# Performance work log

Hardware: AMD Instinct MI355X
Metric: run time of the kernel (lower is better)

The kernel has to match this reference:

```python
import jax, jax.numpy as jnp
import numpy as np

B, T, DIM = 2, 4096, 2048
H, HKV = 16, 4
HD = DIM // H          # 128
NREP = H // HKV        # 4
R = 16                 # csa_compress_ratio
TOPK = 64              # min(csa_top_k, max_seq_len // R)
THETA = 10000.0


def setup_inputs() -> dict:
    key = jax.random.key(0)
    ks = jax.random.split(key, 9)
    s = 0.02
    return {
        "x":   jax.random.normal(ks[0], (B, T, DIM), jnp.float32),
        "wq":  jax.random.normal(ks[1], (DIM, H * HD),  jnp.float32) * s,
        "wk":  jax.random.normal(ks[2], (DIM, HKV * HD), jnp.float32) * s,
        "wv":  jax.random.normal(ks[3], (DIM, HKV * HD), jnp.float32) * s,
        "wo":  jax.random.normal(ks[4], (DIM, DIM), jnp.float32) * s,
        "wiq": jax.random.normal(ks[5], (DIM, HD), jnp.float32) * s,
        "wik": jax.random.normal(ks[6], (DIM, HD), jnp.float32) * s,
        "cwa": jax.random.normal(ks[7], (HD,), jnp.float32) * s,
        "cwb": jax.random.normal(ks[8], (HD,), jnp.float32) * s,
    }


def _rope(x, cos, sin):
    # x: [B, h, T, HD]; pairs (x[2i], x[2i+1]) rotated by angle[t, i]
    half = HD // 2
    xr = x.reshape(*x.shape[:-1], half, 2)
    a, b = xr[..., 0], xr[..., 1]          # [B, h, T, half]
    ra = a * cos - b * sin                 # cos/sin: [T, half] broadcast
    rb = a * sin + b * cos
    return jnp.stack([ra, rb], axis=-1).reshape(x.shape)


def reference(x, wq, wk, wv, wo, wiq, wik, cwa, cwb):
    Bx, Tx, C = x.shape
    half = HD // 2
    # RoPE tables (buffer in original, deterministic -> recomputed here)
    freqs = 1.0 / (THETA ** (jnp.arange(half, dtype=jnp.float32) / half))
    ang = jnp.arange(Tx, dtype=jnp.float32)[:, None] * freqs[None, :]  # [T, half]
    cos, sin = jnp.cos(ang), jnp.sin(ang)

    q = (x @ wq).reshape(Bx, Tx, H, HD).transpose(0, 2, 1, 3)    # [B,H,T,HD]
    k = (x @ wk).reshape(Bx, Tx, HKV, HD).transpose(0, 2, 1, 3)  # [B,HKV,T,HD]
    v = (x @ wv).reshape(Bx, Tx, HKV, HD).transpose(0, 2, 1, 3)
    q = _rope(q, cos, sin)
    k = _rope(k, cos, sin)

    # chunked softmax-weighted KV compression (vectorized over blocks)
    nb = Tx // R
    kb = k.reshape(Bx, HKV, nb, R, HD)
    vb = v.reshape(Bx, HKV, nb, R, HD)
    wa = jax.nn.softmax(kb @ cwa, axis=-1)   # [B,HKV,nb,R], softmax within block
    wb_ = jax.nn.softmax(kb @ cwb, axis=-1)
    w = 0.5 * (wa + wb_)
    ck = jnp.einsum('bhnr,bhnrd->bhnd', w, kb)  # [B,HKV,nb,HD]
    cv = jnp.einsum('bhnr,bhnrd->bhnd', w, vb)

    # indexer: scores[b,t] = mean_j( qi[b,t] . ki[b,j] ) = qi[b,t] . mean_j ki[b,j]
    qi = x @ wiq                         # [B,T,HD]
    ki_mean = (x @ wik).mean(axis=1)     # [B,HD]
    scores = jnp.einsum('btd,bd->bt', qi, ki_mean)  # [B,T]
    block_scores = scores[:, :nb]                   # [B,nb]

    if nb > TOPK:
        idx = jax.lax.top_k(block_scores, TOPK)[1]             # [B,TOPK]
        ck = jnp.take_along_axis(ck, idx[:, None, :, None], axis=2)  # [B,HKV,TOPK,HD]
        cv = jnp.take_along_axis(cv, idx[:, None, :, None], axis=2)

    # GQA repeat + sparse attention over selected compressed blocks (no mask)
    k_rep = jnp.repeat(ck, NREP, axis=1)   # [B,H,TOPK,HD]
    v_rep = jnp.repeat(cv, NREP, axis=1)
    att = jax.nn.softmax(
        jnp.einsum('bhtd,bhsd->bhts', q, k_rep) / jnp.sqrt(jnp.float32(HD)),
        axis=-1)                            # [B,H,T,TOPK]
    out = jnp.einsum('bhts,bhsd->bhtd', att, v_rep)
    out = out.transpose(0, 2, 1, 3).reshape(Bx, Tx, C)
    return out @ wo
```

## Files before the change

### kernel.cpp

```cpp
#include <hip/hip_runtime.h>
#include <math.h>
#include <stdint.h>

#define BB    2
#define TT    4096
#define CDIM  2048
#define NHQ   16
#define NKV   4
#define HD    128
#define HALF  64
#define NREP  4
#define RBLK  16
#define NB    256
#define TOPK  64

#define MROWS (BB * TT)
#define NQKV  (CDIM + 2 * NKV * HD)
#define XELE  ((size_t)MROWS * CDIM)

typedef __bf16 bf16;
typedef __bf16 bf16x4 __attribute__((ext_vector_type(4)));
typedef __bf16 bf16x8 __attribute__((ext_vector_type(8)));
typedef float f32x4 __attribute__((ext_vector_type(4)));

typedef __attribute__((address_space(1))) unsigned int gu32;
typedef __attribute__((address_space(3))) unsigned int lu32;

__device__ __forceinline__ void gload_lds16(const void* g, void* l) {
  void* gv = const_cast<void*>(g);
  __builtin_amdgcn_global_load_lds((gu32*)gv, (lu32*)l, 16, 0, 0);
}


#define LDS_BUF 24576
#define OFF_AL  8192
#define OFF_BH  16384
#define OFF_BL  20480

__device__ __forceinline__ void mfma3_step(const bf16* __restrict__ sb, int arow,
                                           int brow, int chunk, f32x4 acc[4][4]) {
  bf16x8 fah[4], fal[4], fbh[4], fbl[4];
#pragma unroll
  for (int i = 0; i < 4; ++i) {
    fah[i] = *(const bf16x8*)&sb[(arow + i * 16) * 32 + chunk];
    fal[i] = *(const bf16x8*)&sb[OFF_AL + (arow + i * 16) * 32 + chunk];
  }
#pragma unroll
  for (int j = 0; j < 4; ++j) {
    fbh[j] = *(const bf16x8*)&sb[OFF_BH + (brow + j * 16) * 32 + chunk];
    fbl[j] = *(const bf16x8*)&sb[OFF_BL + (brow + j * 16) * 32 + chunk];
  }
  __builtin_amdgcn_s_setprio(1);
#pragma unroll
  for (int j = 0; j < 4; ++j)
#pragma unroll
    for (int i = 0; i < 4; ++i) {
      acc[i][j] = __builtin_amdgcn_mfma_f32_16x16x32_bf16(fah[i], fbh[j], acc[i][j], 0, 0, 0);
      acc[i][j] = __builtin_amdgcn_mfma_f32_16x16x32_bf16(fah[i], fbl[j], acc[i][j], 0, 0, 0);
      acc[i][j] = __builtin_amdgcn_mfma_f32_16x16x32_bf16(fal[i], fbh[j], acc[i][j], 0, 0, 0);
    }
  __builtin_amdgcn_s_setprio(0);
}

__device__ __forceinline__ void mfma3_core8(const bf16* __restrict__ Ah,
                                            const bf16* __restrict__ Al,
                                            const bf16* __restrict__ Bh,
                                            const bf16* __restrict__ Bl,
                                            int bm, int bn,
                                            f32x4 acc[4][4]) {
  __shared__ __align__(16) bf16 smem[2 * LDS_BUF];
  const int tid = threadIdx.x;
  const int wave = tid >> 6, lane = tid & 63;
  const int lr4 = lane >> 2;
  const int cgs = (lane & 3) ^ ((lane >> 3) & 3);
  const size_t stageoff = (size_t)lr4 * CDIM + cgs * 8;

  const bf16* gp[6];
  int loff[6];
#pragma unroll
  for (int u = 0; u < 6; ++u) {
    int c = wave * 6 + u;
    const bf16* base;
    int lbase;
    if (c < 16)      { base = Ah + (size_t)(bm + c * 16) * CDIM;        lbase = c * 512; }
    else if (c < 32) { base = Al + (size_t)(bm + (c - 16) * 16) * CDIM; lbase = OFF_AL + (c - 16) * 512; }
    else if (c < 40) { base = Bh + (size_t)(bn + (c - 32) * 16) * CDIM; lbase = OFF_BH + (c - 32) * 512; }
    else             { base = Bl + (size_t)(bn + (c - 40) * 16) * CDIM; lbase = OFF_BL + (c - 40) * 512; }
    gp[u] = base + stageoff;
    loff[u] = lbase;
  }

  const int wr = wave >> 1, wc = wave & 1;
  const int fr = lane & 15, lg = lane >> 4;
  const int chunk = (lg ^ ((fr >> 1) & 3)) << 3;
  const int arow = wr * 64 + fr;
  const int brow = wc * 64 + fr;

#pragma unroll
  for (int u = 0; u < 6; ++u) gload_lds16(gp[u], &smem[loff[u]]);

  for (int t = 0; t < 63; ++t) {
    const int nbase = ((t + 1) & 1) * LDS_BUF;
    const int kk = (t + 1) * 32;
#pragma unroll
    for (int u = 0; u < 6; ++u) gload_lds16(gp[u] + kk, &smem[nbase + loff[u]]);
    asm volatile("s_waitcnt vmcnt(6)" ::: "memory");
    __builtin_amdgcn_s_barrier();
    asm volatile("" ::: "memory");

    mfma3_step(&smem[(t & 1) * LDS_BUF], arow, brow, chunk, acc);

    asm volatile("" ::: "memory");
    __builtin_amdgcn_s_barrier();
  }
  asm volatile("s_waitcnt vmcnt(0)" ::: "memory");
  __builtin_amdgcn_s_barrier();
  asm volatile("" ::: "memory");
  mfma3_step(&smem[LDS_BUF], arow, brow, chunk, acc);
}

__global__ __launch_bounds__(512, 2) void csa_gemm_qkv(const bf16* __restrict__ xh,
                                                       const bf16* __restrict__ xl,
                                                       const bf16* __restrict__ wth,
                                                       const bf16* __restrict__ wtl,
                                                       float* __restrict__ qb,
                                                       float* __restrict__ kb,
                                                       float* __restrict__ vb) {
  f32x4 acc[4][4] = {};
  const int bm = blockIdx.y << 8, bn = blockIdx.x << 7;
  mfma3_core8(xh, xl, wth, wtl, bm, bn, acc);
  const int wave = threadIdx.x >> 6, lane = threadIdx.x & 63;
  const int wr = wave >> 1, wc = wave & 1;
  const int fr = lane & 15, lg = lane >> 4;
  float* dst; int ncols, colofs;
  if (bn < CDIM)            { dst = qb; ncols = CDIM; colofs = bn; }
  else if (bn < CDIM + 512) { dst = kb; ncols = 512;  colofs = bn - CDIM; }
  else                      { dst = vb; ncols = 512;  colofs = bn - CDIM - 512; }
#pragma unroll
  for (int i = 0; i < 4; ++i)
#pragma unroll
    for (int j = 0; j < 4; ++j) {
      int row0 = bm + wr * 64 + i * 16 + (lg << 2);
      int col = colofs + wc * 64 + j * 16 + fr;
#pragma unroll
      for (int r = 0; r < 4; ++r)
        dst[(size_t)(row0 + r) * ncols + col] = acc[i][j][r];
    }
}

__global__ __launch_bounds__(512, 2) void csa_gemm_wo(const bf16* __restrict__ ah,
                                                      const bf16* __restrict__ al,
                                                      const bf16* __restrict__ wth,
                                                      const bf16* __restrict__ wtl,
                                                      float* __restrict__ C) {
  f32x4 acc[4][4] = {};
  const int bm = blockIdx.y << 8, bn = blockIdx.x << 7;
  mfma3_core8(ah, al, wth, wtl, bm, bn, acc);
  const int wave = threadIdx.x >> 6, lane = threadIdx.x & 63;
  const int wr = wave >> 1, wc = wave & 1;
  const int fr = lane & 15, lg = lane >> 4;
#pragma unroll
  for (int i = 0; i < 4; ++i)
#pragma unroll
    for (int j = 0; j < 4; ++j) {
      int row0 = bm + wr * 64 + i * 16 + (lg << 2);
      int col = bn + wc * 64 + j * 16 + fr;
#pragma unroll
      for (int r = 0; r < 4; ++r)
        C[(size_t)(row0 + r) * CDIM + col] = acc[i][j][r];
    }
}

__global__ void csa_xconv(const float4* __restrict__ x, bf16x4* __restrict__ xh,
                          bf16x4* __restrict__ xl) {
  int i = blockIdx.x * 256 + threadIdx.x;
  float4 v = x[i];
  bf16x4 h, l;
  h[0] = (bf16)v.x; l[0] = (bf16)(v.x - (float)h[0]);
  h[1] = (bf16)v.y; l[1] = (bf16)(v.y - (float)h[1]);
  h[2] = (bf16)v.z; l[2] = (bf16)(v.z - (float)h[2]);
  h[3] = (bf16)v.w; l[3] = (bf16)(v.w - (float)h[3]);
  xh[i] = h;
  xl[i] = l;
}

__global__ __launch_bounds__(256) void csa_wconv(const float* __restrict__ W, int N,
                                                 bf16* __restrict__ wth,
                                                 bf16* __restrict__ wtl, int rowofs) {
  __shared__ float tile[32][33];
  int k0 = blockIdx.y * 32, n0 = blockIdx.x * 32;
  int tx = threadIdx.x & 31, ty = threadIdx.x >> 5;
#pragma unroll
  for (int r = 0; r < 32; r += 8)
    tile[ty + r][tx] = W[(size_t)(k0 + ty + r) * N + n0 + tx];
  __syncthreads();
#pragma unroll
  for (int r = 0; r < 32; r += 8) {
    int n = ty + r;
    float x = tile[tx][n];
    bf16 h = (bf16)x;
    bf16 l = (bf16)(x - (float)h);
    size_t o = (size_t)(rowofs + n0 + n) * CDIM + k0 + tx;
    wth[o] = h;
    wtl[o] = l;
  }
}

__global__ void csa_rope_table(float* __restrict__ cost, float* __restrict__ sint) {
  int idx = blockIdx.x * blockDim.x + threadIdx.x;
  if (idx >= TT * HALF) return;
  int t = idx / HALF, i = idx % HALF;
  double freq = pow(10000.0, -(double)i / (double)HALF);
  double ang = (double)t * freq;
  cost[idx] = (float)cos(ang);
  sint[idx] = (float)sin(ang);
}

__global__ void csa_rope_apply(float* __restrict__ buf, const float* __restrict__ cost,
                               const float* __restrict__ sint, int nheads, int total) {
  int idx = blockIdx.x * blockDim.x + threadIdx.x;
  if (idx >= total) return;
  int i = idx % HALF;
  int h = (idx / HALF) % nheads;
  int t = (idx / (HALF * nheads)) % TT;
  int b = idx / (HALF * nheads * TT);
  float c = cost[t * HALF + i], s = sint[t * HALF + i];
  float* p = buf + ((((size_t)b * TT + t) * nheads + h) * HD) + 2 * i;
  float a = p[0], q = p[1];
  p[0] = a * c - q * s;
  p[1] = a * s + q * c;
}

__global__ void csa_xpart(const float* __restrict__ x, float* __restrict__ xpart) {
  int d = blockIdx.x * 256 + threadIdx.x;
  int ts = blockIdx.y;
  int b = blockIdx.z;
  float s = 0.f;
  int t0 = ts * (TT / 16);
  for (int t = t0; t < t0 + TT / 16; ++t) s += x[((size_t)b * TT + t) * CDIM + d];
  xpart[((size_t)b * 16 + ts) * CDIM + d] = s;
}

__global__ void csa_kimean(const float* __restrict__ xpart, const float* __restrict__ wik,
                           float* __restrict__ ki) {
  int b = blockIdx.x >> 7;
  int j = blockIdx.x & 127;
  int tid = threadIdx.x;
  float s = 0.f;
  for (int d = tid; d < CDIM; d += 256) {
    float xm = 0.f;
#pragma unroll
    for (int ts = 0; ts < 16; ++ts) xm += xpart[((size_t)b * 16 + ts) * CDIM + d];
    s += xm * wik[(size_t)d * HD + j];
  }
  __shared__ float red[256];
  red[tid] = s;
  __syncthreads();
  for (int off = 128; off > 0; off >>= 1) {
    if (tid < off) red[tid] += red[tid + off];
    __syncthreads();
  }
  if (tid == 0) ki[b * HD + j] = red[0] * (1.f / (float)TT);
}

__global__ void csa_u(const float* __restrict__ wiq, const float* __restrict__ ki,
                      float* __restrict__ u) {
  int idx = blockIdx.x * 256 + threadIdx.x;
  int b = idx / CDIM, d = idx % CDIM;
  float s = 0.f;
#pragma unroll 8
  for (int j = 0; j < HD; ++j) s += wiq[(size_t)d * HD + j] * ki[b * HD + j];
  u[idx] = s;
}

__global__ void csa_scores(const float* __restrict__ x, const float* __restrict__ u,
                           float* __restrict__ sc) {
  int b = blockIdx.x >> 8;
  int t = blockIdx.x & 255;
  int tid = threadIdx.x;
  float s = 0.f;
  for (int d = tid; d < CDIM; d += 256)
    s += x[((size_t)b * TT + t) * CDIM + d] * u[b * CDIM + d];
  __shared__ float red[256];
  red[tid] = s;
  __syncthreads();
  for (int off = 128; off > 0; off >>= 1) {
    if (tid < off) red[tid] += red[tid + off];
    __syncthreads();
  }
  if (tid == 0) sc[blockIdx.x] = red[0];
}

__global__ void csa_topk(const float* __restrict__ sc, int* __restrict__ topk) {
  __shared__ float val[NB];
  __shared__ float rv[256];
  __shared__ int ri[256];
  int b = blockIdx.x, tid = threadIdx.x;
  val[tid] = sc[b * NB + tid];
  __syncthreads();
  for (int it = 0; it < TOPK; ++it) {
    rv[tid] = val[tid];
    ri[tid] = tid;
    __syncthreads();
    for (int off = 128; off > 0; off >>= 1) {
      if (tid < off) {
        if (rv[tid + off] > rv[tid] ||
            (rv[tid + off] == rv[tid] && ri[tid + off] < ri[tid])) {
          rv[tid] = rv[tid + off];
          ri[tid] = ri[tid + off];
        }
      }
      __syncthreads();
    }
    if (tid == 0) {
      topk[b * TOPK + it] = ri[0];
      val[ri[0]] = -INFINITY;
    }
    __syncthreads();
  }
}

__global__ __launch_bounds__(64) void csa_compress(const float* __restrict__ kbuf,
                                                   const float* __restrict__ vbuf,
                                                   const int* __restrict__ topk,
                                                   const float* __restrict__ cwa,
                                                   const float* __restrict__ cwb,
                                                   bf16* __restrict__ ckh,
                                                   bf16* __restrict__ ckl,
                                                   bf16* __restrict__ cvth,
                                                   bf16* __restrict__ cvtl) {
  int blk = blockIdx.x;
  int b = blk / (NKV * TOPK);
  int h = (blk / TOPK) % NKV;
  int j = blk % TOPK;
  int n = topk[b * TOPK + j];
  int l = threadIdx.x;
  float ca0 = cwa[l], ca1 = cwa[l + 64];
  float cb0 = cwb[l], cb1 = cwb[l + 64];
  float kk[RBLK][2], vv[RBLK][2], ar[RBLK], br[RBLK];
#pragma unroll
  for (int r = 0; r < RBLK; ++r) {
    int t = n * RBLK + r;
    size_t base = (((size_t)b * TT + t) * NKV + h) * HD;
    kk[r][0] = kbuf[base + l];
    kk[r][1] = kbuf[base + l + 64];
    vv[r][0] = vbuf[base + l];
    vv[r][1] = vbuf[base + l + 64];
    float pa = kk[r][0] * ca0 + kk[r][1] * ca1;
    float pb = kk[r][0] * cb0 + kk[r][1] * cb1;
    for (int off = 32; off > 0; off >>= 1) {
      pa += __shfl_xor(pa, off);
      pb += __shfl_xor(pb, off);
    }
    ar[r] = pa;
    br[r] = pb;
  }
  float ma = -INFINITY, mb = -INFINITY;
#pragma unroll
  for (int r = 0; r < RBLK; ++r) { ma = fmaxf(ma, ar[r]); mb = fmaxf(mb, br[r]); }
  float ea[RBLK], eb[RBLK], sa = 0.f, sb = 0.f;
#pragma unroll
  for (int r = 0; r < RBLK; ++r) {
    ea[r] = expf(ar[r] - ma); sa += ea[r];
    eb[r] = expf(br[r] - mb); sb += eb[r];
  }
  float isa = 1.f / sa, isb = 1.f / sb;
  float o0 = 0.f, o1 = 0.f, p0 = 0.f, p1 = 0.f;
#pragma unroll
  for (int r = 0; r < RBLK; ++r) {
    float w = 0.5f * (ea[r] * isa + eb[r] * isb);
    o0 += w * kk[r][0]; o1 += w * kk[r][1];
    p0 += w * vv[r][0]; p1 += w * vv[r][1];
  }
  size_t ckbase = ((size_t)(b * NKV + h) * 64 + j) * 128;
  bf16 h0 = (bf16)o0; ckh[ckbase + l] = h0;      ckl[ckbase + l] = (bf16)(o0 - (float)h0);
  bf16 h1 = (bf16)o1; ckh[ckbase + l + 64] = h1; ckl[ckbase + l + 64] = (bf16)(o1 - (float)h1);
  size_t vtbase = (size_t)(b * NKV + h) * (128 * 64);
  bf16 g0 = (bf16)p0; cvth[vtbase + (size_t)l * 64 + j] = g0;
  cvtl[vtbase + (size_t)l * 64 + j] = (bf16)(p0 - (float)g0);
  bf16 g1 = (bf16)p1; cvth[vtbase + (size_t)(l + 64) * 64 + j] = g1;
  cvtl[vtbase + (size_t)(l + 64) * 64 + j] = (bf16)(p1 - (float)g1);
}

__global__ __launch_bounds__(256) void csa_attn_mfma(const float* __restrict__ qb,
                                                     const float* __restrict__ cost,
                                                     const float* __restrict__ sint,
                                                     const bf16* __restrict__ ckh_g,
                                                     const bf16* __restrict__ ckl_g,
                                                     const bf16* __restrict__ cvth_g,
                                                     const bf16* __restrict__ cvtl_g,
                                                     bf16* __restrict__ oh_g,
                                                     bf16* __restrict__ ol_g) {
  __shared__ __align__(16) bf16 sck[2][64 * 128];
  __shared__ __align__(16) bf16 sV[2][64 * 64];
  const int tid = threadIdx.x;
  const int wave = tid >> 6, lane = tid & 63;
  const int b = blockIdx.y >> 2, kvh = blockIdx.y & 3;
  const int row0 = blockIdx.x << 7;
  const int wrow = wave << 5;
  const int lr = lane & 15, lg = lane >> 4;
  const float scale = 0.08838834764831845f;

  const bf16* gkh = ckh_g + (size_t)(b * NKV + kvh) * (64 * 128);
  const bf16* gkl = ckl_g + (size_t)(b * NKV + kvh) * (64 * 128);
  const bf16* gvh = cvth_g + (size_t)(b * NKV + kvh) * (128 * 64);
  const bf16* gvl = cvtl_g + (size_t)(b * NKV + kvh) * (128 * 64);

  for (int idx = tid; idx < 1024; idx += 256) {
    int j = idx >> 4, c = idx & 15;
    int dst = (j * 16 + (c ^ (j & 15))) * 8;
    *(uint4*)&sck[0][dst] = *(const uint4*)(gkh + j * 128 + c * 8);
    *(uint4*)&sck[1][dst] = *(const uint4*)(gkl + j * 128 + c * 8);
  }
  for (int idx = tid; idx < 512; idx += 256) {
    int d = idx >> 3, c = idx & 7;
    int dst = (d * 8 + (c ^ (d & 7))) * 8;
    *(uint4*)&sV[0][dst] = *(const uint4*)(gvh + d * 64 + c * 8);
    *(uint4*)&sV[1][dst] = *(const uint4*)(gvl + d * 64 + c * 8);
  }

  bf16x8 qfh[2][4], qfl[2][4];
#pragma unroll
  for (int it = 0; it < 2; ++it)
#pragma unroll
    for (int ks = 0; ks < 4; ++ks) {
      int row = wrow + it * 16 + lr;
      int g = row0 + row;
      int t = g >> 2;
      int hh = kvh * NREP + (g & 3);
      int d0 = ks * 32 + (lg << 3);
      const float* qp = qb + (((size_t)b * TT + t) * NHQ + hh) * HD + d0;
      float4 a = *(const float4*)qp;
      float4 b4 = *(const float4*)(qp + 4);
      float4 cs = *(const float4*)&cost[t * HALF + (d0 >> 1)];
      float4 sn = *(const float4*)&sint[t * HALF + (d0 >> 1)];
      float f[8];
      f[0] = a.x * cs.x - a.y * sn.x;  f[1] = a.x * sn.x + a.y * cs.x;
      f[2] = a.z * cs.y - a.w * sn.y;  f[3] = a.z * sn.y + a.w * cs.y;
      f[4] = b4.x * cs.z - b4.y * sn.z; f[5] = b4.x * sn.z + b4.y * cs.z;
      f[6] = b4.z * cs.w - b4.w * sn.w; f[7] = b4.z * sn.w + b4.w * cs.w;
      bf16x8 h8, l8;
#pragma unroll
      for (int u = 0; u < 8; ++u) {
        h8[u] = (bf16)f[u];
        l8[u] = (bf16)(f[u] - (float)h8[u]);
      }
      qfh[it][ks] = h8;
      qfl[it][ks] = l8;
    }
  __syncthreads();

  f32x4 accS[2][4] = {};
#pragma unroll
  for (int ks = 0; ks < 4; ++ks) {
    bf16x8 kh[4], kl[4];
#pragma unroll
    for (int jt = 0; jt < 4; ++jt) {
      int row = jt * 16 + lr;
      int c = ks * 4 + lg;
      int off = (row * 16 + (c ^ (row & 15))) * 8;
      kh[jt] = *(const bf16x8*)&sck[0][off];
      kl[jt] = *(const bf16x8*)&sck[1][off];
    }
#pragma unroll
    for (int it = 0; it < 2; ++it)
#pragma unroll
      for (int jt = 0; jt < 4; ++jt) {
        accS[it][jt] = __builtin_amdgcn_mfma_f32_16x16x32_bf16(qfh[it][ks], kh[jt], accS[it][jt], 0, 0, 0);
        accS[it][jt] = __builtin_amdgcn_mfma_f32_16x16x32_bf16(qfh[it][ks], kl[jt], accS[it][jt], 0, 0, 0);
        accS[it][jt] = __builtin_amdgcn_mfma_f32_16x16x32_bf16(qfl[it][ks], kh[jt], accS[it][jt], 0, 0, 0);
      }
  }

#pragma unroll
  for (int it = 0; it < 2; ++it)
#pragma unroll
    for (int r = 0; r < 4; ++r) {
      float v0 = accS[it][0][r] * scale, v1 = accS[it][1][r] * scale;
      float v2 = accS[it][2][r] * scale, v3 = accS[it][3][r] * scale;
      float m = fmaxf(fmaxf(v0, v1), fmaxf(v2, v3));
      for (int off = 8; off > 0; off >>= 1) m = fmaxf(m, __shfl_xor(m, off));
      float e0 = expf(v0 - m), e1 = expf(v1 - m), e2 = expf(v2 - m), e3 = expf(v3 - m);
      float s = e0 + e1 + e2 + e3;
      for (int off = 8; off > 0; off >>= 1) s += __shfl_xor(s, off);
      float inv = 1.f / s;
      accS[it][0][r] = e0 * inv; accS[it][1][r] = e1 * inv;
      accS[it][2][r] = e2 * inv; accS[it][3][r] = e3 * inv;
    }

  __syncthreads();

#pragma unroll
  for (int it = 0; it < 2; ++it)
#pragma unroll
    for (int jt = 0; jt < 4; ++jt)
#pragma unroll
      for (int r = 0; r < 4; ++r) {
        int row = wrow + it * 16 + (lg << 2) + r;
        int k = jt * 16 + lr;
        float p = accS[it][jt][r];
        bf16 ph = (bf16)p;
        int c = k >> 3;
        int off = (row * 8 + (c ^ (row & 7))) * 8 + (k & 7);
        sck[0][off] = ph;
        sck[1][off] = (bf16)(p - (float)ph);
      }
  __syncthreads();

  for (int half = 0; half < 2; ++half) {
    if (half) {
      __syncthreads();
      for (int idx = tid; idx < 512; idx += 256) {
        int d = idx >> 3, c = idx & 7;
        int dst = (d * 8 + (c ^ (d & 7))) * 8;
        *(uint4*)&sV[0][dst] = *(const uint4*)(gvh + (64 + d) * 64 + c * 8);
        *(uint4*)&sV[1][dst] = *(const uint4*)(gvl + (64 + d) * 64 + c * 8);
      }
      __syncthreads();
    }
    f32x4 accO[2][4] = {};
#pragma unroll
    for (int ks = 0; ks < 2; ++ks) {
      bf16x8 pah[2], pal[2], vh[4], vl[4];
#pragma unroll
      for (int it = 0; it < 2; ++it) {
        int row = wrow + it * 16 + lr;
        int c = ks * 4 + lg;
        int off = (row * 8 + (c ^ (row & 7))) * 8;
        pah[it] = *(const bf16x8*)&sck[0][off];
        pal[it] = *(const bf16x8*)&sck[1][off];
      }
#pragma unroll
      for (int jt = 0; jt < 4; ++jt) {
        int d = jt * 16 + lr;
        int c = ks * 4 + lg;
        int off = (d * 8 + (c ^ (d & 7))) * 8;
        vh[jt] = *(const bf16x8*)&sV[0][off];
        vl[jt] = *(const bf16x8*)&sV[1][off];
      }
#pragma unroll
      for (int it = 0; it < 2; ++it)
#pragma unroll
        for (int jt = 0; jt < 4; ++jt) {
          accO[it][jt] = __builtin_amdgcn_mfma_f32_16x16x32_bf16(pah[it], vh[jt], accO[it][jt], 0, 0, 0);
          accO[it][jt] = __builtin_amdgcn_mfma_f32_16x16x32_bf16(pah[it], vl[jt], accO[it][jt], 0, 0, 0);
          accO[it][jt] = __builtin_amdgcn_mfma_f32_16x16x32_bf16(pal[it], vh[jt], accO[it][jt], 0, 0, 0);
        }
    }
#pragma unroll
    for (int it = 0; it < 2; ++it)
#pragma unroll
      for (int jt = 0; jt < 4; ++jt)
#pragma unroll
        for (int r = 0; r < 4; ++r) {
          int row = wrow + it * 16 + (lg << 2) + r;
          int g = row0 + row;
          int t = g >> 2;
          int hh = kvh * NREP + (g & 3);
          size_t ob = (((size_t)b * TT + t) * NHQ + hh) * HD + half * 64 + jt * 16 + lr;
          float o = accO[it][jt][r];
          bf16 oh = (bf16)o;
          oh_g[ob] = oh;
          ol_g[ob] = (bf16)(o - (float)oh);
        }
  }
}

extern "C" void kernel_launch(void* const* d_in, const int* in_sizes, int n_in,
                              void* d_out, int out_size, void* d_ws, size_t ws_size,
                              hipStream_t stream) {
  const float* x   = (const float*)d_in[0];
  const float* wq  = (const float*)d_in[1];
  const float* wk  = (const float*)d_in[2];
  const float* wv  = (const float*)d_in[3];
  const float* wo  = (const float*)d_in[4];
  const float* wiq = (const float*)d_in[5];
  const float* wik = (const float*)d_in[6];
  const float* cwa = (const float*)d_in[7];
  const float* cwb = (const float*)d_in[8];
  float* out = (float*)d_out;

  float* qb = out;

  float* ws = (float*)d_ws;
  float* kb   = ws;
  float* vb   = kb + (size_t)MROWS * 512;
  bf16*  xh   = (bf16*)(vb + (size_t)MROWS * 512);
  bf16*  xl   = xh + XELE;
  bf16*  wqh  = xl + XELE;
  bf16*  wql  = wqh + (size_t)NQKV * CDIM;
  float* cost = (float*)(wql + (size_t)NQKV * CDIM);
  float* sint = cost + (size_t)TT * HALF;
  float* xpart = sint + (size_t)TT * HALF;
  float* ki   = xpart + (size_t)BB * 16 * CDIM;
  float* u    = ki + BB * HD;
  float* sc   = u + BB * CDIM;
  bf16*  ckh  = (bf16*)(sc + BB * NB);
  bf16*  ckl  = ckh + (size_t)BB * NKV * 64 * 128;
  bf16*  cvth = ckl + (size_t)BB * NKV * 64 * 128;
  bf16*  cvtl = cvth + (size_t)BB * NKV * 128 * 64;
  int* topk   = (int*)(cvtl + (size_t)BB * NKV * 128 * 64);
  bf16* oh  = xh;
  bf16* ol_ = xl;
  bf16* woh = wqh;
  bf16* wol = wql;

  csa_xconv<<<(XELE / 4) / 256, 256, 0, stream>>>((const float4*)x, (bf16x4*)xh, (bf16x4*)xl);
  csa_wconv<<<dim3(CDIM / 32, CDIM / 32), 256, 0, stream>>>(wq, CDIM, wqh, wql, 0);
  csa_wconv<<<dim3(512 / 32, CDIM / 32), 256, 0, stream>>>(wk, 512, wqh, wql, CDIM);
  csa_wconv<<<dim3(512 / 32, CDIM / 32), 256, 0, stream>>>(wv, 512, wqh, wql, CDIM + 512);

  csa_gemm_qkv<<<dim3(NQKV / 128, MROWS / 256), 512, 0, stream>>>(xh, xl, wqh, wql, qb, kb, vb);

  csa_wconv<<<dim3(CDIM / 32, CDIM / 32), 256, 0, stream>>>(wo, CDIM, woh, wol, 0);

  csa_rope_table<<<(TT * HALF + 255) / 256, 256, 0, stream>>>(cost, sint);
  csa_rope_apply<<<(BB * TT * NKV * HALF + 255) / 256, 256, 0, stream>>>(kb, cost, sint, NKV, BB * TT * NKV * HALF);

  csa_xpart<<<dim3(CDIM / 256, 16, BB), 256, 0, stream>>>(x, xpart);
  csa_kimean<<<BB * HD, 256, 0, stream>>>(xpart, wik, ki);
  csa_u<<<(BB * CDIM) / 256, 256, 0, stream>>>(wiq, ki, u);
  csa_scores<<<BB * NB, 256, 0, stream>>>(x, u, sc);
  csa_topk<<<BB, 256, 0, stream>>>(sc, topk);

  csa_compress<<<BB * NKV * TOPK, 64, 0, stream>>>(kb, vb, topk, cwa, cwb, ckh, ckl, cvth, cvtl);

  csa_attn_mfma<<<dim3((TT * NREP) / 128, BB * NKV), 256, 0, stream>>>(qb, cost, sint, ckh, ckl, cvth, cvtl, oh, ol_);

  csa_gemm_wo<<<dim3(CDIM / 128, MROWS / 256), 512, 0, stream>>>(oh, ol_, woh, wol, out);
}
```

Measured before the change: 804.9 us.

## Interleave GEMM global-to-LDS prefetch with per-column MFMA phases and add XCD swizzle

```diff
diff --git a/kernel.cpp b/kernel.cpp
--- a/kernel.cpp
+++ b/kernel.cpp
@@ -31,43 +31,20 @@
   __builtin_amdgcn_global_load_lds((gu32*)gv, (lu32*)l, 16, 0, 0);
 }
 
+#define MFMA_BF16 __builtin_amdgcn_mfma_f32_16x16x32_bf16
+
 
 #define LDS_BUF 24576
 #define OFF_AL  8192
 #define OFF_BH  16384
 #define OFF_BL  20480
 
-__device__ __forceinline__ void mfma3_step(const bf16* __restrict__ sb, int arow,
-                                           int brow, int chunk, f32x4 acc[4][4]) {
-  bf16x8 fah[4], fal[4], fbh[4], fbl[4];
-#pragma unroll
-  for (int i = 0; i < 4; ++i) {
-    fah[i] = *(const bf16x8*)&sb[(arow + i * 16) * 32 + chunk];
-    fal[i] = *(const bf16x8*)&sb[OFF_AL + (arow + i * 16) * 32 + chunk];
-  }
-#pragma unroll
-  for (int j = 0; j < 4; ++j) {
-    fbh[j] = *(const bf16x8*)&sb[OFF_BH + (brow + j * 16) * 32 + chunk];
-    fbl[j] = *(const bf16x8*)&sb[OFF_BL + (brow + j * 16) * 32 + chunk];
-  }
-  __builtin_amdgcn_s_setprio(1);
-#pragma unroll
-  for (int j = 0; j < 4; ++j)
-#pragma unroll
-    for (int i = 0; i < 4; ++i) {
-      acc[i][j] = __builtin_amdgcn_mfma_f32_16x16x32_bf16(fah[i], fbh[j], acc[i][j], 0, 0, 0);
-      acc[i][j] = __builtin_amdgcn_mfma_f32_16x16x32_bf16(fah[i], fbl[j], acc[i][j], 0, 0, 0);
-      acc[i][j] = __builtin_amdgcn_mfma_f32_16x16x32_bf16(fal[i], fbh[j], acc[i][j], 0, 0, 0);
-    }
-  __builtin_amdgcn_s_setprio(0);
-}
-
-__device__ __forceinline__ void mfma3_core8(const bf16* __restrict__ Ah,
-                                            const bf16* __restrict__ Al,
-                                            const bf16* __restrict__ Bh,
-                                            const bf16* __restrict__ Bl,
-                                            int bm, int bn,
-                                            f32x4 acc[4][4]) {
+__device__ __forceinline__ void mfma3_core8p(const bf16* __restrict__ Ah,
+                                             const bf16* __restrict__ Al,
+                                             const bf16* __restrict__ Bh,
+                                             const bf16* __restrict__ Bl,
+                                             int bm, int bn,
+                                             f32x4 acc[4][4]) {
   __shared__ __align__(16) bf16 smem[2 * LDS_BUF];
   const int tid = threadIdx.x;
   const int wave = tid >> 6, lane = tid & 63;
@@ -81,13 +58,13 @@
   for (int u = 0; u < 6; ++u) {
     int c = wave * 6 + u;
     const bf16* base;
-    int lbase;
-    if (c < 16)      { base = Ah + (size_t)(bm + c * 16) * CDIM;        lbase = c * 512; }
-    else if (c < 32) { base = Al + (size_t)(bm + (c - 16) * 16) * CDIM; lbase = OFF_AL + (c - 16) * 512; }
-    else if (c < 40) { base = Bh + (size_t)(bn + (c - 32) * 16) * CDIM; lbase = OFF_BH + (c - 32) * 512; }
-    else             { base = Bl + (size_t)(bn + (c - 40) * 16) * CDIM; lbase = OFF_BL + (c - 40) * 512; }
+    int lb;
+    if (c < 16)      { base = Ah + (size_t)(bm + c * 16) * CDIM;        lb = c * 512; }
+    else if (c < 32) { base = Al + (size_t)(bm + (c - 16) * 16) * CDIM; lb = OFF_AL + (c - 16) * 512; }
+    else if (c < 40) { base = Bh + (size_t)(bn + (c - 32) * 16) * CDIM; lb = OFF_BH + (c - 32) * 512; }
+    else             { base = Bl + (size_t)(bn + (c - 40) * 16) * CDIM; lb = OFF_BL + (c - 40) * 512; }
     gp[u] = base + stageoff;
-    loff[u] = lbase;
+    loff[u] = lb;
   }
 
   const int wr = wave >> 1, wc = wave & 1;
@@ -99,24 +76,77 @@
 #pragma unroll
   for (int u = 0; u < 6; ++u) gload_lds16(gp[u], &smem[loff[u]]);
 
-  for (int t = 0; t < 63; ++t) {
-    const int nbase = ((t + 1) & 1) * LDS_BUF;
+  for (int t = 0; t < 64; ++t) {
+    const bf16* cb = &smem[(t & 1) * LDS_BUF];
+    bf16* nb = &smem[((t + 1) & 1) * LDS_BUF];
     const int kk = (t + 1) * 32;
-#pragma unroll
-    for (int u = 0; u < 6; ++u) gload_lds16(gp[u] + kk, &smem[nbase + loff[u]]);
-    asm volatile("s_waitcnt vmcnt(6)" ::: "memory");
+    const bool nlast = (t < 63);
+
+    if (nlast) {
+      gload_lds16(gp[0] + kk, nb + loff[0]);
+      gload_lds16(gp[1] + kk, nb + loff[1]);
+      asm volatile("s_waitcnt vmcnt(2)" ::: "memory");
+    } else {
+      asm volatile("s_waitcnt vmcnt(0)" ::: "memory");
+    }
     __builtin_amdgcn_s_barrier();
     asm volatile("" ::: "memory");
 
-    mfma3_step(&smem[(t & 1) * LDS_BUF], arow, brow, chunk, acc);
-
+    bf16x8 fah[4], fal[4];
+#pragma unroll
+    for (int i = 0; i < 4; ++i) {
+      fah[i] = *(const bf16x8*)&cb[(arow + i * 16) * 32 + chunk];
+      fal[i] = *(const bf16x8*)&cb[OFF_AL + (arow + i * 16) * 32 + chunk];
+    }
+    {
+      bf16x8 fbh = *(const bf16x8*)&cb[OFF_BH + brow * 32 + chunk];
+      bf16x8 fbl = *(const bf16x8*)&cb[OFF_BL + brow * 32 + chunk];
+      __builtin_amdgcn_s_setprio(1);
+#pragma unroll
+      for (int i = 0; i < 4; ++i) {
+        acc[i][0] = MFMA_BF16(fah[i], fbh, acc[i][0], 0, 0, 0);
+        acc[i][0] = MFMA_BF16(fah[i], fbl, acc[i][0], 0, 0, 0);
+        acc[i][0] = MFMA_BF16(fal[i], fbh, acc[i][0], 0, 0, 0);
+      }
+      __builtin_amdgcn_s_setprio(0);
+    }
     asm volatile("" ::: "memory");
     __builtin_amdgcn_s_barrier();
-  }
-  asm volatile("s_waitcnt vmcnt(0)" ::: "memory");
-  __builtin_amdgcn_s_barrier();
-  asm volatile("" ::: "memory");
-  mfma3_step(&smem[LDS_BUF], arow, brow, chunk, acc);
+    asm volatile("" ::: "memory");
+
+#pragma unroll
+    for (int j = 1; j < 4; ++j) {
+      if (nlast && j < 3) {
+        gload_lds16(gp[2 * j] + kk, nb + loff[2 * j]);
+        gload_lds16(gp[2 * j + 1] + kk, nb + loff[2 * j + 1]);
+      }
+      bf16x8 fbh = *(const bf16x8*)&cb[OFF_BH + (brow + j * 16) * 32 + chunk];
+      bf16x8 fbl = *(const bf16x8*)&cb[OFF_BL + (brow + j * 16) * 32 + chunk];
+      asm volatile("" ::: "memory");
+      __builtin_amdgcn_s_barrier();
+      __builtin_amdgcn_s_setprio(1);
+#pragma unroll
+      for (int i = 0; i < 4; ++i) {
+        acc[i][j] = MFMA_BF16(fah[i], fbh, acc[i][j], 0, 0, 0);
+        acc[i][j] = MFMA_BF16(fah[i], fbl, acc[i][j], 0, 0, 0);
+        acc[i][j] = MFMA_BF16(fal[i], fbh, acc[i][j], 0, 0, 0);
+      }
+      __builtin_amdgcn_s_setprio(0);
+      asm volatile("" ::: "memory");
+      __builtin_amdgcn_s_barrier();
+      asm volatile("" ::: "memory");
+    }
+  }
+}
+
+__device__ __forceinline__ void xcd_swizzle(int& by, int& bx) {
+  const int nwgx = gridDim.x;
+  const int nwg = nwgx * gridDim.y;
+  const int cpx = nwg >> 3;
+  const int bid = blockIdx.y * nwgx + blockIdx.x;
+  const int l = (bid & 7) * cpx + (bid >> 3);
+  by = l / nwgx;
+  bx = l - by * nwgx;
 }
 
 __global__ __launch_bounds__(512, 2) void csa_gemm_qkv(const bf16* __restrict__ xh,
@@ -127,8 +157,10 @@
                                                        float* __restrict__ kb,
                                                        float* __restrict__ vb) {
   f32x4 acc[4][4] = {};
-  const int bm = blockIdx.y << 8, bn = blockIdx.x << 7;
-  mfma3_core8(xh, xl, wth, wtl, bm, bn, acc);
+  int by, bx;
+  xcd_swizzle(by, bx);
+  const int bm = by << 8, bn = bx << 7;
+  mfma3_core8p(xh, xl, wth, wtl, bm, bn, acc);
   const int wave = threadIdx.x >> 6, lane = threadIdx.x & 63;
   const int wr = wave >> 1, wc = wave & 1;
   const int fr = lane & 15, lg = lane >> 4;
@@ -154,8 +186,10 @@
                                                       const bf16* __restrict__ wtl,
                                                       float* __restrict__ C) {
   f32x4 acc[4][4] = {};
-  const int bm = blockIdx.y << 8, bn = blockIdx.x << 7;
-  mfma3_core8(ah, al, wth, wtl, bm, bn, acc);
+  int by, bx;
+  xcd_swizzle(by, bx);
+  const int bm = by << 8, bn = bx << 7;
+  mfma3_core8p(ah, al, wth, wtl, bm, bn, acc);
   const int wave = threadIdx.x >> 6, lane = threadIdx.x & 63;
   const int wr = wave >> 1, wc = wave & 1;
   const int fr = lane & 15, lg = lane >> 4;
@@ -466,9 +500,9 @@
     for (int it = 0; it < 2; ++it)
 #pragma unroll
       for (int jt = 0; jt < 4; ++jt) {
-        accS[it][jt] = __builtin_amdgcn_mfma_f32_16x16x32_bf16(qfh[it][ks], kh[jt], accS[it][jt], 0, 0, 0);
-        accS[it][jt] = __builtin_amdgcn_mfma_f32_16x16x32_bf16(qfh[it][ks], kl[jt], accS[it][jt], 0, 0, 0);
-        accS[it][jt] = __builtin_amdgcn_mfma_f32_16x16x32_bf16(qfl[it][ks], kh[jt], accS[it][jt], 0, 0, 0);
+        accS[it][jt] = MFMA_BF16(qfh[it][ks], kh[jt], accS[it][jt], 0, 0, 0);
+        accS[it][jt] = MFMA_BF16(qfh[it][ks], kl[jt], accS[it][jt], 0, 0, 0);
+        accS[it][jt] = MFMA_BF16(qfl[it][ks], kh[jt], accS[it][jt], 0, 0, 0);
       }
   }
 
@@ -542,9 +576,9 @@
       for (int it = 0; it < 2; ++it)
 #pragma unroll
         for (int jt = 0; jt < 4; ++jt) {
-          accO[it][jt] = __builtin_amdgcn_mfma_f32_16x16x32_bf16(pah[it], vh[jt], accO[it][jt], 0, 0, 0);
-          accO[it][jt] = __builtin_amdgcn_mfma_f32_16x16x32_bf16(pah[it], vl[jt], accO[it][jt], 0, 0, 0);
-          accO[it][jt] = __builtin_amdgcn_mfma_f32_16x16x32_bf16(pal[it], vh[jt], accO[it][jt], 0, 0, 0);
+          accO[it][jt] = MFMA_BF16(pah[it], vh[jt], accO[it][jt], 0, 0, 0);
+          accO[it][jt] = MFMA_BF16(pah[it], vl[jt], accO[it][jt], 0, 0, 0);
+          accO[it][jt] = MFMA_BF16(pal[it], vh[jt], accO[it][jt], 0, 0, 0);
         }
     }
 #pragma unroll
```

Result: faster. 773.7 us (-3.9%).
